# Performance work log

Hardware: AMD Instinct MI355X
Metric: run time of the kernel (lower is better)

Reference implementation:

```python
import jax, jax.numpy as jnp
import numpy as np

H = 16
D = 64
WIN = 512
THETA = 10000.0


def _rope(x):
    # x: [B, H, T, D]
    T = x.shape[2]
    inv = 1.0 / (THETA ** (jnp.arange(0, D, 2, dtype=jnp.float32) / D))  # [D/2]
    f = jnp.arange(T, dtype=jnp.float32)[:, None] * inv[None, :]          # [T, D/2]
    f = jnp.concatenate([f, f], axis=-1)                                  # [T, D]
    cos, sin = jnp.cos(f), jnp.sin(f)
    x1, x2 = jnp.split(x, 2, axis=-1)
    rot = jnp.concatenate([-x2, x1], axis=-1)
    return x * cos + rot * sin


def setup_inputs() -> dict:
    key = jax.random.key(0)
    ks = jax.random.split(key, 9)
    C = H * D
    s = 0.02
    return {
        "x":  jax.random.normal(ks[0], (2, 2048, C), dtype=jnp.float32),
        "Wq": jax.random.normal(ks[1], (C, C), dtype=jnp.float32) * s,
        "bq": jnp.zeros((C,), dtype=jnp.float32),
        "Wk": jax.random.normal(ks[2], (C, C), dtype=jnp.float32) * s,
        "bk": jnp.zeros((C,), dtype=jnp.float32),
        "Wv": jax.random.normal(ks[3], (C, C), dtype=jnp.float32) * s,
        "bv": jnp.zeros((C,), dtype=jnp.float32),
        "Wo": jax.random.normal(ks[4], (C, C), dtype=jnp.float32) * s,
        "bo": jnp.zeros((C,), dtype=jnp.float32),
    }


def reference(x, Wq, bq, Wk, bk, Wv, bv, Wo, bo):
    B, T, C = x.shape
    def split_heads(y):
        return y.reshape(B, T, H, D).transpose(0, 2, 1, 3)  # [B,H,T,D]
    q = split_heads(x @ Wq + bq)
    k = split_heads(x @ Wk + bk)
    v = split_heads(x @ Wv + bv)
    q = _rope(q)
    k = _rope(k)
    scores = jnp.einsum('bhqd,bhkd->bhqk', q, k) * (1.0 / np.sqrt(D))
    # the original module does NOT apply a causal mask, only the window).
    idx = jnp.arange(T)
    allowed = idx[None, :] >= idx[:, None] - (WIN - 1)      # [T, T] bool
    scores = jnp.where(allowed[None, None], scores, -jnp.inf)
    attn = jax.nn.softmax(scores, axis=-1)
    out = jnp.einsum('bhqk,bhkd->bhqd', attn, v)
    out = out.transpose(0, 2, 1, 3).reshape(B, T, C)
    return out @ Wo + bo
```

## Files before the change

### kernel.cpp

```cpp
#include <hip/hip_runtime.h>
#include <hip/hip_bf16.h>
#include <math.h>

#define Bsz 2
#define Tt  2048
#define Cc  1024
#define Hh  16
#define Dd  64

typedef __attribute__((ext_vector_type(8))) short short8v;
typedef __attribute__((ext_vector_type(4))) short short4v;
typedef __attribute__((ext_vector_type(8))) _Float16 half8v;
typedef __attribute__((ext_vector_type(4))) float f32x4;
typedef __attribute__((ext_vector_type(16))) float f32x16;
typedef __attribute__((ext_vector_type(4))) unsigned int uint4v;

static __device__ __forceinline__ short f2h(float f) {
  _Float16 h = (_Float16)f;
  return __builtin_bit_cast(short, h);
}
static __device__ __forceinline__ float h2f(short s) {
  _Float16 h = __builtin_bit_cast(_Float16, s);
  return (float)h;
}
static __device__ __forceinline__ void gll16(const void* g, void* l) {
  __builtin_amdgcn_global_load_lds((const __attribute__((address_space(1))) unsigned int*)g,
                                   (__attribute__((address_space(3))) unsigned int*)l, 16, 0, 0);
}

__global__ void cast_x(const float* __restrict__ x, short* __restrict__ xh) {
  int t = blockIdx.x * 256 + threadIdx.x;
  const float* s = x + (size_t)t * 8;
  float4 a = *(const float4*)s, b = *(const float4*)(s + 4);
  short8v h;
  h[0] = f2h(a.x); h[1] = f2h(a.y); h[2] = f2h(a.z); h[3] = f2h(a.w);
  h[4] = f2h(b.x); h[5] = f2h(b.y); h[6] = f2h(b.z); h[7] = f2h(b.w);
  *(short8v*)(xh + (size_t)t * 8) = h;
}

__global__ __launch_bounds__(256) void cast_wT(const float* __restrict__ Wq,
                                               const float* __restrict__ Wk,
                                               const float* __restrict__ Wv,
                                               const float* __restrict__ Wo,
                                               short* __restrict__ WTh) {
  __shared__ float T[64][68];
  const int z = blockIdx.z;
  const float* W = z == 0 ? Wq : z == 1 ? Wk : z == 2 ? Wv : Wo;
  short* oh = WTh + (size_t)z * 1048576;
  const int n0 = blockIdx.x * 64, k0 = blockIdx.y * 64;
  const int tid = threadIdx.x;
#pragma unroll
  for (int i = 0; i < 4; ++i) {
    int slot = tid + i * 256;
    int r = slot >> 4, c4 = (slot & 15) << 2;
    *(float4*)&T[r][c4] = *(const float4*)(W + (size_t)(k0 + r) * Cc + n0 + c4);
  }
  __syncthreads();
#pragma unroll
  for (int i = 0; i < 2; ++i) {
    int slot = tid + i * 256;
    int nl = slot >> 3, ks = (slot & 7) << 3;
    short8v h;
#pragma unroll
    for (int e = 0; e < 8; ++e) h[e] = f2h(T[ks + e][nl]);
    *(short8v*)(oh + (size_t)(n0 + nl) * Cc + k0 + ks) = h;
  }
}

__device__ __forceinline__ void core128h(const short* __restrict__ Ah,
                                         const short* __restrict__ Bh,
                                         short* AhL, short* BhL,
                                         int row0, int col0, int wv, int lane, f32x4 acc[4][4]) {
  const int l15 = lane & 15, g = lane >> 4;
  const int wr = wv >> 1, wc = wv & 1;

  const int r8 = lane >> 3;
  const int sch = ((lane & 7) ^ r8) << 3;
  size_t aoff[4], boff[4];
#pragma unroll
  for (int gi = 0; gi < 4; ++gi) {
    aoff[gi] = (size_t)(row0 + wv * 32 + 8 * gi + r8) * Cc + sch;
    boff[gi] = (size_t)(col0 + wv * 32 + 8 * gi + r8) * Cc + sch;
  }
  short* dA = AhL + wv * 2048;
  short* dB = BhL + wv * 2048;

  int aL[4][2], bL[4][2];
#pragma unroll
  for (int m = 0; m < 4; ++m)
#pragma unroll
    for (int s = 0; s < 2; ++s) {
      aL[m][s] = (wr * 64 + m * 16 + l15) * 64 + (((4 * s + g) ^ (l15 & 7)) << 3);
      bL[m][s] = (wc * 64 + m * 16 + l15) * 64 + (((4 * s + g) ^ (l15 & 7)) << 3);
    }

  for (int k0 = 0; k0 < Cc; k0 += 64) {
    __syncthreads();
#pragma unroll
    for (int gi = 0; gi < 4; ++gi) {
      gll16(Ah + aoff[gi] + k0, dA + gi * 512);
      gll16(Bh + boff[gi] + k0, dB + gi * 512);
    }
    __syncthreads();
#pragma unroll
    for (int s = 0; s < 2; ++s) {
      half8v a[4], b[4];
#pragma unroll
      for (int m = 0; m < 4; ++m) a[m] = __builtin_bit_cast(half8v, *(short8v*)&AhL[aL[m][s]]);
#pragma unroll
      for (int n = 0; n < 4; ++n) b[n] = __builtin_bit_cast(half8v, *(short8v*)&BhL[bL[n][s]]);
#pragma unroll
      for (int m = 0; m < 4; ++m)
#pragma unroll
        for (int n = 0; n < 4; ++n)
          acc[m][n] = __builtin_amdgcn_mfma_f32_16x16x32_f16(a[m], b[n], acc[m][n], 0, 0, 0);
    }
  }
}

__global__ __launch_bounds__(256, 3) void gemm_qkv(const short* __restrict__ xh,
                                                   const short* __restrict__ WTh,
                                                   const float* __restrict__ bq,
                                                   const float* __restrict__ bk,
                                                   const float* __restrict__ bv,
                                                   short* __restrict__ qb,
                                                   short* __restrict__ kb,
                                                   short* __restrict__ vb) {
  __shared__ short AhL[8192], BhL[8192];
  const int mode = blockIdx.y;
  const short* Bh = WTh + (size_t)mode * 1048576;
  const float* bias = mode == 0 ? bq : mode == 1 ? bk : bv;
  short* Y = mode == 0 ? qb : mode == 1 ? kb : vb;

  const int bid = blockIdx.x;
  const int nid = ((bid & 7) << 5) | (bid >> 3);
  const int row0 = (nid >> 3) * 128, col0 = (nid & 7) * 128;
  const int lane = threadIdx.x & 63, wv = threadIdx.x >> 6;
  const int l15 = lane & 15, g = lane >> 4;
  const int wr = wv >> 1, wc = wv & 1;

  f32x4 acc[4][4];
#pragma unroll
  for (int m = 0; m < 4; ++m)
#pragma unroll
    for (int n = 0; n < 4; ++n) acc[m][n] = (f32x4){0.f, 0.f, 0.f, 0.f};

  core128h(xh, Bh, AhL, BhL, row0, col0, wv, lane, acc);

  const int cbase = col0 + wc * 64;
  const int h = cbase >> 6;
  if (mode < 2) {
    const float scale = (mode == 0) ? 0.18033688f : 1.0f;
#pragma unroll
    for (int n = 0; n < 2; ++n) {
      const int d = n * 16 + l15;
      const float b0 = bias[cbase + d], b1 = bias[cbase + d + 32];
      const float inv = exp2f(-(float)d * (13.2877123795494f / 32.f));
#pragma unroll
      for (int m = 0; m < 4; ++m)
#pragma unroll
        for (int rr = 0; rr < 4; ++rr) {
          int R = row0 + wr * 64 + m * 16 + g * 4 + rr;
          int bI = R >> 11, t = R & (Tt - 1);
          float sn, cs;
          sincosf((float)t * inv, &sn, &cs);
          float v0 = acc[m][n][rr] + b0, v1 = acc[m][n + 2][rr] + b1;
          size_t base = (((size_t)(bI * Hh + h) * Tt + t) << 6) + d;
          Y[base]      = f2h((v0 * cs - v1 * sn) * scale);
          Y[base + 32] = f2h((v1 * cs + v0 * sn) * scale);
        }
    }
  } else {
#pragma unroll
    for (int n = 0; n < 2; ++n) {
      const int d = n * 16 + l15;
      const float b0 = bias[cbase + d], b1 = bias[cbase + d + 32];
#pragma unroll
      for (int m = 0; m < 4; ++m) {
        int R = row0 + wr * 64 + m * 16 + g * 4;
        int bI = R >> 11, t = R & (Tt - 1);
        short4v s0, s1;
#pragma unroll
        for (int rr = 0; rr < 4; ++rr) {
          s0[rr] = f2h(acc[m][n][rr] + b0);
          s1[rr] = f2h(acc[m][n + 2][rr] + b1);
        }
        size_t base = ((size_t)(bI * Hh + h) * Dd);
        *(short4v*)(Y + (base + d) * Tt + t)      = s0;
        *(short4v*)(Y + (base + d + 32) * Tt + t) = s1;
      }
    }
  }
}

__global__ __launch_bounds__(256, 3) void gemm_out(const short* __restrict__ ah,
                                                   const short* __restrict__ WTo,
                                                   const float* __restrict__ bias,
                                                   float* __restrict__ Y) {
  __shared__ short AhL[8192], BhL[8192];
  const int bid = blockIdx.x;
  const int nid = ((bid & 7) << 5) | (bid >> 3);
  const int row0 = (nid >> 3) * 128, col0 = (nid & 7) * 128;
  const int lane = threadIdx.x & 63, wv = threadIdx.x >> 6;
  const int l15 = lane & 15, g = lane >> 4;
  const int wr = wv >> 1, wc = wv & 1;

  f32x4 acc[4][4];
#pragma unroll
  for (int m = 0; m < 4; ++m)
#pragma unroll
    for (int n = 0; n < 4; ++n) acc[m][n] = (f32x4){0.f, 0.f, 0.f, 0.f};

  core128h(ah, WTo, AhL, BhL, row0, col0, wv, lane, acc);

  const int cbase = col0 + wc * 64;
#pragma unroll
  for (int n = 0; n < 2; ++n) {
    const int ccol = cbase + n * 16 + l15;
    const float b0 = bias[ccol], b1 = bias[ccol + 32];
#pragma unroll
    for (int m = 0; m < 4; ++m)
#pragma unroll
      for (int rr = 0; rr < 4; ++rr) {
        int R = row0 + wr * 64 + m * 16 + g * 4 + rr;
        Y[(size_t)R * Cc + ccol]      = acc[m][n][rr] + b0;
        Y[(size_t)R * Cc + ccol + 32] = acc[m][n + 2][rr] + b1;
      }
  }
}

static __device__ const int JQ[27] = {11, 0,0, 1,1, 2,2, 3,3, 4,4, 12, 5,5,
                                      6,6, 13, 7,7, 8,8, 14, 9,9, 15, 10,10};
static __device__ const int JK[27] = {0, 0,1, 0,1, 0,1, 0,1, 0,1, 0, 0,1,
                                      0,1, 0, 0,1, 0,1, 0, 0,1, 0, 0,1};

__global__ __launch_bounds__(256, 4) void attn_mfma(const short* __restrict__ q,
                                                    const short* __restrict__ k,
                                                    const short* __restrict__ vT,
                                                    short* __restrict__ ah,
                                                    float* __restrict__ yb,
                                                    float* __restrict__ side) {
  const int n = blockIdx.x;
  const int xcd = n & 7;
  const int t7 = n >> 3;
  const int bhj = t7 / 27;
  const int j = t7 - bhj * 27;
  const int bh = xcd * 4 + bhj;
  const int Q = JQ[j];
  const int kh = JK[j];
  const int split = (Q <= 10);
  const int q0 = Q * 128;

  const int tid = threadIdx.x;
  const int lane = tid & 63;
  const int wv = tid >> 6;
  const int l31 = lane & 31;
  const int hb = lane >> 5;
  const int qbase = q0 + wv * 32;
  const int tq = qbase + l31;

  const short* qgb = q + (size_t)bh * Tt * Dd;
  const short* kgb = k + (size_t)bh * Tt * Dd;
  const short* vgb = vT + (size_t)bh * Dd * Tt;

  const short* qp = qgb + (size_t)tq * Dd + 8 * hb;
  half8v qf[4];
#pragma unroll
  for (int i = 0; i < 4; ++i) qf[i] = __builtin_bit_cast(half8v, *(const short8v*)(qp + 16 * i));

  __shared__ short Klds[2][4096];
  __shared__ short Vt[2][4096];

  const int r8 = lane >> 3;
  const size_t ksrc0 = (size_t)(wv * 16 + r8) * Dd + (((lane & 7) ^ r8) << 3);
  const size_t ksrc1 = ksrc0 + (size_t)8 * Dd;
  const int vlog = ((lane & 7) - r8) & 7;
  const size_t vsrc0 = (size_t)(wv * 16 + r8) * Tt + (vlog << 3);
  const size_t vsrc1 = vsrc0 + (size_t)8 * Tt;

#define STAGE64(BUF, JT)                                                     \
  {                                                                          \
    gll16(kgb + (size_t)(JT) * Dd + ksrc0, &Klds[BUF][wv * 1024]);           \
    gll16(kgb + (size_t)(JT) * Dd + ksrc1, &Klds[BUF][wv * 1024 + 512]);     \
    gll16(vgb + vsrc0 + (JT), &Vt[BUF][wv * 1024]);                          \
    gll16(vgb + vsrc1 + (JT), &Vt[BUF][wv * 1024 + 512]);                    \
  }

  int koff[4], voff[4];
#pragma unroll
  for (int i = 0; i < 4; ++i) {
    koff[i] = l31 * 64 + (((2 * i + hb) ^ (l31 & 7)) << 3);
    voff[i] = l31 * 64 + ((((2 * i + hb) + (l31 & 7)) & 7) << 3);
  }

  f32x16 oacc[2];
#pragma unroll
  for (int t = 0; t < 2; ++t)
#pragma unroll
    for (int r = 0; r < 16; ++r) oacc[t][r] = 0.f;
  float lrun = 0.f;

  const int cs0 = (q0 >= 512) ? (q0 - 511) : 0;
  const int cstart = cs0 & ~63;
  const int nch_b = (Tt - cstart) >> 6;
  const int lower = (nch_b + 1) >> 1;
  const int mystart = cstart + ((split && kh) ? (lower << 6) : 0);
  const int myn = split ? (kh ? nch_b - lower : lower) : nch_b;

  STAGE64(0, mystart);
  __syncthreads();

  int cur = 0;
  for (int ci = 0; ci < myn; ++ci) {
    const int jt = mystart + (ci << 6);

    if (ci + 1 < myn) STAGE64(cur ^ 1, jt + 64);

    const short* kbuf = &Klds[cur][0];
    f32x16 seA, seB;
#pragma unroll
    for (int r = 0; r < 16; ++r) { seA[r] = 0.f; seB[r] = 0.f; }
    __builtin_amdgcn_s_setprio(1);
#pragma unroll
    for (int i = 0; i < 4; ++i) {
      half8v kfA = __builtin_bit_cast(half8v, *(short8v*)&kbuf[koff[i]]);
      seA = __builtin_amdgcn_mfma_f32_32x32x16_f16(kfA, qf[i], seA, 0, 0, 0);
    }
#pragma unroll
    for (int i = 0; i < 4; ++i) {
      half8v kfB = __builtin_bit_cast(half8v, *(short8v*)&kbuf[koff[i] + 2048]);
      seB = __builtin_amdgcn_mfma_f32_32x32x16_f16(kfB, qf[i], seB, 0, 0, 0);
    }
    __builtin_amdgcn_s_setprio(0);

    if (jt < qbase - 480) {
      int th = tq - 511 - jt;
#pragma unroll
      for (int r = 0; r < 16; ++r) {
        int row = (r & 3) + 8 * (r >> 2) + 4 * hb;
        if (row < th) seA[r] = -1e30f;
        if (32 + row < th) seB[r] = -1e30f;
      }
    }

    float pA[16], pB[16];
#pragma unroll
    for (int r = 0; r < 16; ++r) {
      asm("v_exp_f32 %0, %1" : "=v"(pA[r]) : "v"(seA[r]));
      asm("v_exp_f32 %0, %1" : "=v"(pB[r]) : "v"(seB[r]));
    }
    float t0 = 0.f, t1 = 0.f, t2 = 0.f, t3 = 0.f;
#pragma unroll
    for (int r = 0; r < 16; r += 4) {
      t0 += pA[r];     t1 += pA[r + 1]; t2 += pA[r + 2]; t3 += pA[r + 3];
      t0 += pB[r];     t1 += pB[r + 1]; t2 += pB[r + 2]; t3 += pB[r + 3];
    }
    float psum = (t0 + t1) + (t2 + t3);
    psum += __shfl_xor(psum, 32);
    lrun += psum;

    unsigned pa[8], pb[8];
#pragma unroll
    for (int i = 0; i < 8; ++i) {
      pa[i] = __builtin_bit_cast(unsigned, __builtin_amdgcn_cvt_pkrtz(pA[2 * i], pA[2 * i + 1]));
      pb[i] = __builtin_bit_cast(unsigned, __builtin_amdgcn_cvt_pkrtz(pB[2 * i], pB[2 * i + 1]));
    }
    asm volatile("v_permlane32_swap_b32 %0, %1" : "+v"(pa[0]), "+v"(pa[2]));
    asm volatile("v_permlane32_swap_b32 %0, %1" : "+v"(pa[1]), "+v"(pa[3]));
    asm volatile("v_permlane32_swap_b32 %0, %1" : "+v"(pa[4]), "+v"(pa[6]));
    asm volatile("v_permlane32_swap_b32 %0, %1" : "+v"(pa[5]), "+v"(pa[7]));
    asm volatile("v_permlane32_swap_b32 %0, %1" : "+v"(pb[0]), "+v"(pb[2]));
    asm volatile("v_permlane32_swap_b32 %0, %1" : "+v"(pb[1]), "+v"(pb[3]));
    asm volatile("v_permlane32_swap_b32 %0, %1" : "+v"(pb[4]), "+v"(pb[6]));
    asm volatile("v_permlane32_swap_b32 %0, %1" : "+v"(pb[5]), "+v"(pb[7]));
    uint4v fA0, fA1, fB0, fB1;
    fA0[0] = pa[0]; fA0[1] = pa[1]; fA0[2] = pa[2]; fA0[3] = pa[3];
    fA1[0] = pa[4]; fA1[1] = pa[5]; fA1[2] = pa[6]; fA1[3] = pa[7];
    fB0[0] = pb[0]; fB0[1] = pb[1]; fB0[2] = pb[2]; fB0[3] = pb[3];
    fB1[0] = pb[4]; fB1[1] = pb[5]; fB1[2] = pb[6]; fB1[3] = pb[7];
    half8v pfA0 = __builtin_bit_cast(half8v, fA0);
    half8v pfA1 = __builtin_bit_cast(half8v, fA1);
    half8v pfB0 = __builtin_bit_cast(half8v, fB0);
    half8v pfB1 = __builtin_bit_cast(half8v, fB1);

    const short* vbuf = &Vt[cur][0];
    __builtin_amdgcn_s_setprio(1);
#pragma unroll
    for (int t = 0; t < 2; ++t) {
      const int ro = t * 2048;
      half8v v0 = __builtin_bit_cast(half8v, *(short8v*)&vbuf[voff[0] + ro]);
      half8v v1 = __builtin_bit_cast(half8v, *(short8v*)&vbuf[voff[1] + ro]);
      half8v v2 = __builtin_bit_cast(half8v, *(short8v*)&vbuf[voff[2] + ro]);
      half8v v3 = __builtin_bit_cast(half8v, *(short8v*)&vbuf[voff[3] + ro]);
      oacc[t] = __builtin_amdgcn_mfma_f32_32x32x16_f16(v0, pfA0, oacc[t], 0, 0, 0);
      oacc[t] = __builtin_amdgcn_mfma_f32_32x32x16_f16(v1, pfA1, oacc[t], 0, 0, 0);
      oacc[t] = __builtin_amdgcn_mfma_f32_32x32x16_f16(v2, pfB0, oacc[t], 0, 0, 0);
      oacc[t] = __builtin_amdgcn_mfma_f32_32x32x16_f16(v3, pfB1, oacc[t], 0, 0, 0);
    }
    __builtin_amdgcn_s_setprio(0);

    __syncthreads();
    cur ^= 1;
  }

  const float invl = 1.f / lrun;
  const int row = bh * Tt + tq;
  if (split && hb == 0) side[kh * 65536 + row] = lrun;
  const int bI = bh >> 4, hd = bh & 15;
  if (!split || kh == 0) {
    short* op = ah + ((size_t)(bI * Tt + tq)) * Cc + hd * Dd;
#pragma unroll
    for (int t = 0; t < 2; ++t)
#pragma unroll
      for (int rq = 0; rq < 4; ++rq) {
        short4v hv;
#pragma unroll
        for (int rr = 0; rr < 4; ++rr) hv[rr] = f2h(oacc[t][4 * rq + rr] * invl);
        *(short4v*)(op + 32 * t + 8 * rq + 4 * hb) = hv;
      }
  } else {
    float* yp = yb + (size_t)row * 64;
#pragma unroll
    for (int t = 0; t < 2; ++t)
#pragma unroll
      for (int rq = 0; rq < 4; ++rq) {
        f32x4 o4;
#pragma unroll
        for (int rr = 0; rr < 4; ++rr) o4[rr] = oacc[t][4 * rq + rr] * invl;
        *(f32x4*)(yp + 32 * t + 8 * rq + 4 * hb) = o4;
      }
  }
}

__global__ __launch_bounds__(256) void attn_merge(short* __restrict__ ah,
                                                  const float* __restrict__ yb,
                                                  const float* __restrict__ side) {
  const int bh = blockIdx.y;
  const int idx = blockIdx.x * 256 + threadIdx.x;
  const int tq = idx >> 2;
  const int qd = (idx & 3) << 4;
  const int row = bh * Tt + tq;
  const float l0 = side[row], l1 = side[65536 + row];
  const float inv = 1.f / (l0 + l1);
  const float a0 = l0 * inv, a1 = l1 * inv;

  const int bI = bh >> 4, hd = bh & 15;
  short* op = ah + ((size_t)(bI * Tt + tq)) * Cc + hd * Dd + qd;
  const float* yp = yb + (size_t)row * 64 + qd;

  short8v h0 = *(short8v*)op, h1 = *(short8v*)(op + 8);
  short8v o0, o1;
#pragma unroll
  for (int e = 0; e < 8; ++e) o0[e] = f2h(a0 * h2f(h0[e]) + a1 * yp[e]);
#pragma unroll
  for (int e = 0; e < 8; ++e) o1[e] = f2h(a0 * h2f(h1[e]) + a1 * yp[8 + e]);
  *(short8v*)op = o0;
  *(short8v*)(op + 8) = o1;
}

extern "C" void kernel_launch(void* const* d_in, const int* in_sizes, int n_in,
                              void* d_out, int out_size, void* d_ws, size_t ws_size,
                              hipStream_t stream) {
  const float* x  = (const float*)d_in[0];
  const float* Wq = (const float*)d_in[1];
  const float* bq = (const float*)d_in[2];
  const float* Wk = (const float*)d_in[3];
  const float* bk = (const float*)d_in[4];
  const float* Wv = (const float*)d_in[5];
  const float* bv = (const float*)d_in[6];
  const float* Wo = (const float*)d_in[7];
  const float* bo = (const float*)d_in[8];

  short* ws16 = (short*)d_ws;
  short* xh  = ws16;
  short* WTh = ws16 + 4194304;
  short* qb  = ws16 + 8388608;
  short* kb  = ws16 + 12582912;
  short* vb  = ws16 + 16777216;
  short* ah  = ws16 + 20971520;
  float* yb   = (float*)(ws16 + 25165824);
  float* side = yb + 4194304;

  cast_x<<<2048, 256, 0, stream>>>(x, xh);
  cast_wT<<<dim3(16, 16, 4), 256, 0, stream>>>(Wq, Wk, Wv, Wo, WTh);

  gemm_qkv<<<dim3(256, 3), 256, 0, stream>>>(xh, WTh, bq, bk, bv, qb, kb, vb);

  attn_mfma<<<864, 256, 0, stream>>>(qb, kb, vb, ah, yb, side);
  attn_merge<<<dim3(22, 32), 256, 0, stream>>>(ah, yb, side);

  gemm_out<<<256, 256, 0, stream>>>(ah, WTh + 3 * 1048576, bo, (float*)d_out);
}
```

Baseline: 118.9 us.

## Merge cast kernels into one prep launch and precompute RoPE table

Replaces the separate x-cast and weight-transpose-cast kernels with a single prep kernel whose block ranges handle x, the weights, and a new cos/sin table for RoPE. The QKV GEMM epilogue then reads cos/sin from that table instead of calling sincosf per element. This removes one kernel launch and the transcendental math from the GEMM epilogue, at the cost of extra global reads of a 2048x32 float2 table. The __syncthreads now sits inside a block-uniform branch, which is safe.

Measured after the change: 117.9 us. No clear change (-0.9%).

```diff
diff --git a/kernel.cpp b/kernel.cpp
--- a/kernel.cpp
+++ b/kernel.cpp
@@ -28,42 +28,56 @@
                                    (__attribute__((address_space(3))) unsigned int*)l, 16, 0, 0);
 }
 
-__global__ void cast_x(const float* __restrict__ x, short* __restrict__ xh) {
-  int t = blockIdx.x * 256 + threadIdx.x;
-  const float* s = x + (size_t)t * 8;
-  float4 a = *(const float4*)s, b = *(const float4*)(s + 4);
-  short8v h;
-  h[0] = f2h(a.x); h[1] = f2h(a.y); h[2] = f2h(a.z); h[3] = f2h(a.w);
-  h[4] = f2h(b.x); h[5] = f2h(b.y); h[6] = f2h(b.z); h[7] = f2h(b.w);
-  *(short8v*)(xh + (size_t)t * 8) = h;
-}
-
-__global__ __launch_bounds__(256) void cast_wT(const float* __restrict__ Wq,
-                                               const float* __restrict__ Wk,
-                                               const float* __restrict__ Wv,
-                                               const float* __restrict__ Wo,
-                                               short* __restrict__ WTh) {
+__global__ __launch_bounds__(256) void prep(const float* __restrict__ x,
+                                            const float* __restrict__ Wq,
+                                            const float* __restrict__ Wk,
+                                            const float* __restrict__ Wv,
+                                            const float* __restrict__ Wo,
+                                            short* __restrict__ xh,
+                                            short* __restrict__ WTh,
+                                            float* __restrict__ rt) {
   __shared__ float T[64][68];
-  const int z = blockIdx.z;
-  const float* W = z == 0 ? Wq : z == 1 ? Wk : z == 2 ? Wv : Wo;
-  short* oh = WTh + (size_t)z * 1048576;
-  const int n0 = blockIdx.x * 64, k0 = blockIdx.y * 64;
+  const int bid = blockIdx.x;
   const int tid = threadIdx.x;
-#pragma unroll
-  for (int i = 0; i < 4; ++i) {
-    int slot = tid + i * 256;
-    int r = slot >> 4, c4 = (slot & 15) << 2;
-    *(float4*)&T[r][c4] = *(const float4*)(W + (size_t)(k0 + r) * Cc + n0 + c4);
-  }
-  __syncthreads();
-#pragma unroll
-  for (int i = 0; i < 2; ++i) {
-    int slot = tid + i * 256;
-    int nl = slot >> 3, ks = (slot & 7) << 3;
+
+  if (bid < 2048) {
+    int t = bid * 256 + tid;
+    const float* s = x + (size_t)t * 8;
+    float4 a = *(const float4*)s, b = *(const float4*)(s + 4);
     short8v h;
-#pragma unroll
-    for (int e = 0; e < 8; ++e) h[e] = f2h(T[ks + e][nl]);
-    *(short8v*)(oh + (size_t)(n0 + nl) * Cc + k0 + ks) = h;
+    h[0] = f2h(a.x); h[1] = f2h(a.y); h[2] = f2h(a.z); h[3] = f2h(a.w);
+    h[4] = f2h(b.x); h[5] = f2h(b.y); h[6] = f2h(b.z); h[7] = f2h(b.w);
+    *(short8v*)(xh + (size_t)t * 8) = h;
+  } else if (bid < 3072) {
+    const int z = (bid - 2048) >> 8;
+    const int slot = (bid - 2048) & 255;
+    const float* W = z == 0 ? Wq : z == 1 ? Wk : z == 2 ? Wv : Wo;
+    short* oh = WTh + (size_t)z * 1048576;
+    const int n0 = (slot & 15) * 64, k0 = (slot >> 4) * 64;
+#pragma unroll
+    for (int i = 0; i < 4; ++i) {
+      int s2 = tid + i * 256;
+      int r = s2 >> 4, c4 = (s2 & 15) << 2;
+      *(float4*)&T[r][c4] = *(const float4*)(W + (size_t)(k0 + r) * Cc + n0 + c4);
+    }
+    __syncthreads();
+#pragma unroll
+    for (int i = 0; i < 2; ++i) {
+      int s2 = tid + i * 256;
+      int nl = s2 >> 3, ks = (s2 & 7) << 3;
+      short8v h;
+#pragma unroll
+      for (int e = 0; e < 8; ++e) h[e] = f2h(T[ks + e][nl]);
+      *(short8v*)(oh + (size_t)(n0 + nl) * Cc + k0 + ks) = h;
+    }
+  } else {
+    int idx = (bid - 3072) * 256 + tid;
+    int t = idx >> 5, p = idx & 31;
+    float inv = exp2f(-(float)p * (13.2877123795494f / 32.f));
+    float sn, cs;
+    sincosf((float)t * inv, &sn, &cs);
+    float2 v; v.x = cs; v.y = sn;
+    *(float2*)(rt + (size_t)idx * 2) = v;
   }
 }
 
@@ -123,6 +137,7 @@
                                                    const float* __restrict__ bq,
                                                    const float* __restrict__ bk,
                                                    const float* __restrict__ bv,
+                                                   const float* __restrict__ rt,
                                                    short* __restrict__ qb,
                                                    short* __restrict__ kb,
                                                    short* __restrict__ vb) {
@@ -151,23 +166,22 @@
   const int h = cbase >> 6;
   if (mode < 2) {
     const float scale = (mode == 0) ? 0.18033688f : 1.0f;
+    const float2* rt2 = (const float2*)rt;
 #pragma unroll
     for (int n = 0; n < 2; ++n) {
       const int d = n * 16 + l15;
       const float b0 = bias[cbase + d], b1 = bias[cbase + d + 32];
-      const float inv = exp2f(-(float)d * (13.2877123795494f / 32.f));
 #pragma unroll
       for (int m = 0; m < 4; ++m)
 #pragma unroll
         for (int rr = 0; rr < 4; ++rr) {
           int R = row0 + wr * 64 + m * 16 + g * 4 + rr;
           int bI = R >> 11, t = R & (Tt - 1);
-          float sn, cs;
-          sincosf((float)t * inv, &sn, &cs);
+          float2 cssn = rt2[t * 32 + d];
           float v0 = acc[m][n][rr] + b0, v1 = acc[m][n + 2][rr] + b1;
           size_t base = (((size_t)(bI * Hh + h) * Tt + t) << 6) + d;
-          Y[base]      = f2h((v0 * cs - v1 * sn) * scale);
-          Y[base + 32] = f2h((v1 * cs + v0 * sn) * scale);
+          Y[base]      = f2h((v0 * cssn.x - v1 * cssn.y) * scale);
+          Y[base + 32] = f2h((v1 * cssn.x + v0 * cssn.y) * scale);
         }
     }
   } else {
@@ -480,11 +494,11 @@
   short* ah  = ws16 + 20971520;
   float* yb   = (float*)(ws16 + 25165824);
   float* side = yb + 4194304;
-
-  cast_x<<<2048, 256, 0, stream>>>(x, xh);
-  cast_wT<<<dim3(16, 16, 4), 256, 0, stream>>>(Wq, Wk, Wv, Wo, WTh);
-
-  gemm_qkv<<<dim3(256, 3), 256, 0, stream>>>(xh, WTh, bq, bk, bv, qb, kb, vb);
+  float* rt   = side + 131072;
+
+  prep<<<3328, 256, 0, stream>>>(x, Wq, Wk, Wv, Wo, xh, WTh, rt);
+
+  gemm_qkv<<<dim3(256, 3), 256, 0, stream>>>(xh, WTh, bq, bk, bv, rt, qb, kb, vb);
 
   attn_mfma<<<864, 256, 0, stream>>>(qb, kb, vb, ah, yb, side);
   attn_merge<<<dim3(22, 32), 256, 0, stream>>>(ah, yb, side);
```
